# Kernel optimization log

Measured on AMD Instinct MI355X. Metric: run time of the kernel, lower is better.

The kernel has to match this reference:

```python
import jax, jax.numpy as jnp
import numpy as np

N_NODES = 50000
N_EDGES = 800000
N_GRAPHS = 128
F_IN = 128
HID = 64
EDGE_DIM = 16
H1, H2 = 4, 2
NEG_SLOPE = 0.2


def _glorot(key, shape, fan_in):
    return jax.random.normal(key, shape, dtype=jnp.float32) / np.sqrt(fan_in)


def setup_inputs() -> dict:
    key = jax.random.key(0)
    ks = jax.random.split(key, 20)
    x = jax.random.normal(ks[0], (N_NODES, F_IN), dtype=jnp.float32)
    edge_attr = jax.random.normal(ks[1], (N_EDGES, EDGE_DIM), dtype=jnp.float32)
    edge_index = jax.random.randint(ks[2], (2, N_EDGES), 0, N_NODES, dtype=jnp.int32)
    # evenly spread graph ids so every graph is non-empty (sorted)
    batch = (jnp.arange(N_NODES, dtype=jnp.int32) * N_GRAPHS) // N_NODES
    p = {
        'W1': _glorot(ks[3], (F_IN, H1 * HID), F_IN),
        'a_src1': _glorot(ks[4], (H1, HID), HID),
        'a_dst1': _glorot(ks[5], (H1, HID), HID),
        'We1': _glorot(ks[6], (EDGE_DIM, H1 * HID), EDGE_DIM),
        'a_e1': _glorot(ks[7], (H1, HID), HID),
        'b1': jnp.zeros((H1 * HID,), jnp.float32),
        'W2': _glorot(ks[8], (H1 * HID, H2 * HID), H1 * HID),
        'a_src2': _glorot(ks[9], (H2, HID), HID),
        'a_dst2': _glorot(ks[10], (H2, HID), HID),
        'We2': _glorot(ks[11], (EDGE_DIM, H2 * HID), EDGE_DIM),
        'a_e2': _glorot(ks[12], (H2, HID), HID),
        'b2': jnp.zeros((HID,), jnp.float32),
        'Wr': _glorot(ks[13], (HID, 1), HID),
        'br': jnp.zeros((1,), jnp.float32),
    }
    return dict(x=x, edge_attr=edge_attr, edge_index=edge_index, batch=batch, **p)


def _segment_softmax(scores, seg, num_segments):
    # scores: [E, H], softmax grouped by seg (destination node)
    m = jax.ops.segment_max(scores, seg, num_segments)
    m = jnp.where(jnp.isfinite(m), m, 0.0)
    ex = jnp.exp(scores - m[seg])
    s = jax.ops.segment_sum(ex, seg, num_segments)
    return ex / (s[seg] + 1e-16)


def _add_self_loops(edge_index, edge_attr, n):
    # PyG add_self_loops with fill_value='mean': per-dst mean of edge_attr
    src, dst = edge_index[0], edge_index[1]
    cnt = jax.ops.segment_sum(jnp.ones((src.shape[0],), jnp.float32), dst, n)
    loop_attr = jax.ops.segment_sum(edge_attr, dst, n) / jnp.maximum(cnt, 1.0)[:, None]
    loop = jnp.arange(n, dtype=src.dtype)
    return (jnp.concatenate([src, loop]), jnp.concatenate([dst, loop]),
            jnp.concatenate([edge_attr, loop_attr], axis=0))


def _gat_layer(x, e_attr, src, dst, W, a_src, a_dst, We, a_e, b, heads, outc, concat):
    n = x.shape[0]
    xs = (x @ W).reshape(n, heads, outc)                 # [N,H,C]
    s_src = jnp.einsum('nhc,hc->nh', xs, a_src)
    s_dst = jnp.einsum('nhc,hc->nh', xs, a_dst)
    ee = (e_attr @ We).reshape(-1, heads, outc)          # [E,H,C]
    s_e = jnp.einsum('ehc,hc->eh', ee, a_e)
    score = jax.nn.leaky_relu(s_src[src] + s_dst[dst] + s_e, NEG_SLOPE)  # [E,H]
    alpha = _segment_softmax(score, dst, n)
    out = jax.ops.segment_sum(xs[src] * alpha[..., None], dst, n)        # [N,H,C]
    out = out.reshape(n, heads * outc) if concat else out.mean(axis=1)
    return out + b


def reference(x, edge_attr, edge_index, batch,
              W1, a_src1, a_dst1, We1, a_e1, b1,
              W2, a_src2, a_dst2, We2, a_e2, b2, Wr, br):
    n = x.shape[0]
    src, dst, ea = _add_self_loops(edge_index, edge_attr, n)
    h = _gat_layer(x, ea, src, dst, W1, a_src1, a_dst1, We1, a_e1, b1, H1, HID, True)
    h = jax.nn.relu(h)
    h = _gat_layer(h, ea, src, dst, W2, a_src2, a_dst2, We2, a_e2, b2, H2, HID, False)
    g = jax.ops.segment_max(h, batch, N_GRAPHS)          # global max pool [G, HID]
    return g @ Wr + br
```

## Files before the change

kernel.cpp:

```cpp
#include <hip/hip_runtime.h>
#include <hip/hip_bf16.h>
#include <hip/hip_fp16.h>

#define DEVINL __device__ __forceinline__
typedef __hip_bfloat16 bf16;

typedef __attribute__((ext_vector_type(8))) __bf16 bf16x8;
typedef __attribute__((ext_vector_type(4))) float f32x4;

static constexpr int N_NODES  = 50000;
static constexpr int N_EDGES  = 800000;
static constexpr int N_GRAPHS = 128;
static constexpr float NEG_SLOPE = 0.2f;

DEVINL float ldIn(const void* __restrict__ p, size_t i, int isbf) {
    if (isbf) return __bfloat162float(((const bf16*)p)[i]);
    return ((const float*)p)[i];
}

DEVINL unsigned short f2bf(float f) {
    bf16 b = __float2bfloat16(f);
    return *reinterpret_cast<unsigned short*>(&b);
}

DEVINL unsigned f2hbits(float f) {
    __half h = __float2half(f);
    return (unsigned)*reinterpret_cast<unsigned short*>(&h);
}

DEVINL float hbits2f(unsigned bits) {
    unsigned short us = (unsigned short)bits;
    __half h = *reinterpret_cast<__half*>(&us);
    return __half2float(h);
}

DEVINL float lrelu_exp(float sc) {
    sc = sc > 0.f ? sc : NEG_SLOPE * sc;
    return __expf(sc);
}

DEVINL void accw(float w, unsigned wv, float& a0, float& a1) {
    a0 = fmaf(w, __uint_as_float(wv << 16), a0);
    a1 = fmaf(w, __uint_as_float(wv & 0xffff0000u), a1);
}

template<int H>
DEVINL float getse(const uint4& rv, int h) {
    unsigned bits;
    if (H == 4) {
        unsigned w16 = (h & 2) ? rv.z : rv.y;
        bits = (h & 1) ? (w16 >> 16) : (w16 & 0xffffu);
    } else {
        bits = h ? (rv.w >> 16) : (rv.w & 0xffffu);
    }
    return hbits2f(bits);
}

template<int K, int M>
DEVINL void wfrag_build(const void* __restrict__ W, int isbf,
                        bf16* __restrict__ Wfrag, int idx)
{
    constexpr int KS = K / 32;
    constexpr int total = (M / 16) * KS * 64 * 8;
    if (idx >= total) return;
    int j    = idx & 7;
    int lane = (idx >> 3) & 63;
    int rem  = idx >> 9;
    int ks   = rem % KS;
    int ct   = rem / KS;
    int k = ks * 32 + (lane >> 4) * 8 + j;
    int n = ct * 16 + (lane & 15);
    Wfrag[idx] = __float2bfloat16(ldIn(W, (size_t)k * M + n, isbf));
}

__global__ __launch_bounds__(256)
void prep_kernel(const unsigned short* __restrict__ xu,
                 const void* __restrict__ We1, const void* __restrict__ ae1,
                 const void* __restrict__ We2, const void* __restrict__ ae2,
                 const void* __restrict__ W1,  const void* __restrict__ W2,
                 int* __restrict__ flagp,
                 float* __restrict__ M1, float* __restrict__ M2,
                 bf16* __restrict__ wf1, bf16* __restrict__ wf2)
{
    __shared__ int sflag;
    const int bx = blockIdx.x;
    const int t  = threadIdx.x;
    if (t < 64) {
        int bad = 0;
        for (int i = t; i < 1024; i += 64) {
            unsigned u = xu[2 * i];
            float v = __uint_as_float(u << 16);
            if (!(fabsf(v) <= 1e4f)) bad = 1;
        }
        unsigned long long m = __ballot(bad);
        if (t == 0) sflag = m ? 0 : 1;
    }
    __syncthreads();
    const int isbf = sflag;
    if (bx == 0 && t == 0) *flagp = isbf;

    if (bx == 0) {
        if (t < 64) {
            int d = t >> 2, h = t & 3;
            float s = 0.f;
            for (int c = 0; c < 64; ++c)
                s += ldIn(We1, d * 256 + h * 64 + c, isbf) * ldIn(ae1, h * 64 + c, isbf);
            M1[d * 4 + h] = s;
        }
        if (t < 32) {
            int d = t >> 1, h = t & 1;
            float s = 0.f;
            for (int c = 0; c < 64; ++c)
                s += ldIn(We2, d * 128 + h * 64 + c, isbf) * ldIn(ae2, h * 64 + c, isbf);
            M2[d * 2 + h] = s;
        }
    } else if (bx <= 128) {
        wfrag_build<128, 256>(W1, isbf, wf1, (bx - 1) * 256 + t);
    } else {
        wfrag_build<256, 128>(W2, isbf, wf2, (bx - 129) * 256 + t);
    }
}

template<int K, int M, int AMODE, int H>
__global__ __launch_bounds__(256)
void gemm_mfma_kernel(const void* __restrict__ A, const bf16* __restrict__ Wfrag,
                      bf16* __restrict__ C, const int* __restrict__ flagp, int N,
                      const void* __restrict__ a_src, const void* __restrict__ a_dst,
                      float* __restrict__ sA, float* __restrict__ sD)
{
    constexpr int KS = K / 32, CT = M / 16;
    constexpr int LDA = K + 8;
    __shared__ __align__(16) unsigned short Asm[64 * LDA];
    const int isbf = *flagp;
    const int tid  = threadIdx.x;
    const int wave = tid >> 6, lane = tid & 63;
    const int n0 = blockIdx.x * 64;

    for (int i = tid; i < 64 * (K / 8); i += 256) {
        int r  = i / (K / 8);
        int kc = (i % (K / 8)) * 8;
        int n  = n0 + r;
        unsigned short v[8] = {0, 0, 0, 0, 0, 0, 0, 0};
        if (n < N) {
            size_t base = (size_t)n * K + kc;
            if (AMODE == 1 || isbf) {
                *reinterpret_cast<uint4*>(v) =
                    *reinterpret_cast<const uint4*>((const unsigned short*)A + base);
            } else {
                const float* Af = (const float*)A + base;
                float4 f0 = *reinterpret_cast<const float4*>(Af);
                float4 f1 = *reinterpret_cast<const float4*>(Af + 4);
                v[0] = f2bf(f0.x); v[1] = f2bf(f0.y); v[2] = f2bf(f0.z); v[3] = f2bf(f0.w);
                v[4] = f2bf(f1.x); v[5] = f2bf(f1.y); v[6] = f2bf(f1.z); v[7] = f2bf(f1.w);
            }
        }
        *reinterpret_cast<uint4*>(&Asm[r * LDA + kc]) = *reinterpret_cast<uint4*>(v);
    }
    __syncthreads();

    f32x4 acc[CT];
    #pragma unroll
    for (int ct = 0; ct < CT; ++ct) acc[ct] = (f32x4){0.f, 0.f, 0.f, 0.f};

    const int arow  = wave * 16 + (lane & 15);
    const int akoff = (lane >> 4) * 8;
    #pragma unroll
    for (int ks = 0; ks < KS; ++ks) {
        bf16x8 af = *reinterpret_cast<const bf16x8*>(&Asm[arow * LDA + ks * 32 + akoff]);
        #pragma unroll
        for (int ct = 0; ct < CT; ++ct) {
            bf16x8 bfr = *reinterpret_cast<const bf16x8*>(
                &Wfrag[(((size_t)ct * KS + ks) * 64 + lane) * 8]);
            acc[ct] = __builtin_amdgcn_mfma_f32_16x16x32_bf16(af, bfr, acc[ct], 0, 0, 0);
        }
    }

    const int crow0 = n0 + wave * 16 + (lane >> 4) * 4;
    const int ccol  = lane & 15;
    #pragma unroll
    for (int ct = 0; ct < CT; ++ct) {
        #pragma unroll
        for (int r = 0; r < 4; ++r) {
            int row = crow0 + r;
            if (row < N) C[(size_t)row * M + ct * 16 + ccol] = __float2bfloat16(acc[ct][r]);
        }
    }

    float psA[4][H], psD[4][H];
    #pragma unroll
    for (int r = 0; r < 4; ++r)
        #pragma unroll
        for (int hh = 0; hh < H; ++hh) { psA[r][hh] = 0.f; psD[r][hh] = 0.f; }
    #pragma unroll
    for (int ct = 0; ct < CT; ++ct) {
        float as = ldIn(a_src, ct * 16 + ccol, isbf);
        float ad = ldIn(a_dst, ct * 16 + ccol, isbf);
        const int hh = ct >> 2;
        #pragma unroll
        for (int r = 0; r < 4; ++r) {
            psA[r][hh] += acc[ct][r] * as;
            psD[r][hh] += acc[ct][r] * ad;
        }
    }
    #pragma unroll
    for (int m = 1; m < 16; m <<= 1) {
        #pragma unroll
        for (int r = 0; r < 4; ++r)
            #pragma unroll
            for (int hh = 0; hh < H; ++hh) {
                psA[r][hh] += __shfl_xor(psA[r][hh], m);
                psD[r][hh] += __shfl_xor(psD[r][hh], m);
            }
    }
    if (ccol == 0) {
        #pragma unroll
        for (int r = 0; r < 4; ++r) {
            int row = crow0 + r;
            if (row < N) {
                #pragma unroll
                for (int hh = 0; hh < H; ++hh) {
                    sA[(size_t)row * H + hh] = psA[r][hh];
                    sD[(size_t)row * H + hh] = psD[r][hh];
                }
            }
        }
    }
}

__global__ void csr_count_kernel(const int* __restrict__ dst, int* __restrict__ cnt,
                                 int* __restrict__ rank)
{
    int e = blockIdx.x * blockDim.x + threadIdx.x;
    if (e >= N_EDGES) return;
    rank[e] = atomicAdd(&cnt[dst[e]], 1);
}

__global__ __launch_bounds__(256)
void scan_sum_kernel(const int* __restrict__ cnt, int* __restrict__ bsum)
{
    __shared__ int sm[256];
    int i = blockIdx.x * 256 + threadIdx.x;
    sm[threadIdx.x] = (i < N_NODES) ? cnt[i] : 0;
    __syncthreads();
    for (int off = 128; off; off >>= 1) {
        if (threadIdx.x < off) sm[threadIdx.x] += sm[threadIdx.x + off];
        __syncthreads();
    }
    if (threadIdx.x == 0) bsum[blockIdx.x] = sm[0];
}

__global__ __launch_bounds__(256)
void scan_off_kernel(int* __restrict__ bsum, int nb)
{
    __shared__ int sm[256];
    int tid = threadIdx.x;
    int v = (tid < nb) ? bsum[tid] : 0;
    sm[tid] = v;
    __syncthreads();
    for (int off = 1; off < 256; off <<= 1) {
        int t = (tid >= off) ? sm[tid - off] : 0;
        __syncthreads();
        sm[tid] += t;
        __syncthreads();
    }
    if (tid < nb) bsum[tid] = sm[tid] - v;
}

__global__ __launch_bounds__(256)
void scan_final_kernel(const int* __restrict__ cnt, const int* __restrict__ bsum,
                       int* __restrict__ row)
{
    __shared__ int sm[256];
    int i = blockIdx.x * 256 + threadIdx.x;
    int tid = threadIdx.x;
    int v = (i < N_NODES) ? cnt[i] : 0;
    sm[tid] = v;
    __syncthreads();
    for (int off = 1; off < 256; off <<= 1) {
        int t = (tid >= off) ? sm[tid - off] : 0;
        __syncthreads();
        sm[tid] += t;
        __syncthreads();
    }
    int excl = sm[tid] - v + bsum[blockIdx.x];
    if (i < N_NODES) row[i] = excl;
    if (i == N_NODES - 1) row[N_NODES] = excl + v;
}

__global__ void csr_scatter_kernel(const int* __restrict__ srcI, const int* __restrict__ dstI,
                                   const void* __restrict__ eattr, const int* __restrict__ flagp,
                                   const float* __restrict__ M1, const float* __restrict__ M2,
                                   const int* __restrict__ row, const int* __restrict__ rank,
                                   uint4* __restrict__ erec)
{
    const int isbf = *flagp;
    int e = blockIdx.x * blockDim.x + threadIdx.x;
    if (e >= N_EDGES) return;
    float attr[16];
    #pragma unroll
    for (int k = 0; k < 16; ++k) attr[k] = ldIn(eattr, (size_t)e * 16 + k, isbf);
    float4 o1 = {0.f, 0.f, 0.f, 0.f};
    float2 o2 = {0.f, 0.f};
    #pragma unroll
    for (int k = 0; k < 16; ++k) {
        o1.x += attr[k] * M1[k * 4 + 0];
        o1.y += attr[k] * M1[k * 4 + 1];
        o1.z += attr[k] * M1[k * 4 + 2];
        o1.w += attr[k] * M1[k * 4 + 3];
        o2.x += attr[k] * M2[k * 2 + 0];
        o2.y += attr[k] * M2[k * 2 + 1];
    }
    int pos = row[dstI[e]] + rank[e];
    uint4 rec;
    rec.x = (unsigned)srcI[e];
    rec.y = f2hbits(o1.x) | (f2hbits(o1.y) << 16);
    rec.z = f2hbits(o1.z) | (f2hbits(o1.w) << 16);
    rec.w = f2hbits(o2.x) | (f2hbits(o2.y) << 16);
    erec[pos] = rec;
}

template<int H, int LAYER>
__global__ __launch_bounds__(256)
void agg_fused_kernel(const int* __restrict__ row, const uint4* __restrict__ erec,
                      const bf16* __restrict__ xs,
                      const float* __restrict__ sA, const float* __restrict__ sD,
                      const void* __restrict__ bias,
                      const int* __restrict__ flagp, void* __restrict__ out)
{
    constexpr int C   = H * 64;
    constexpr int CPL = C / 16;
    constexpr int NQ  = CPL / 8;
    const int isbf = *flagp;
    int dv = (blockIdx.x * 256 + threadIdx.x) >> 6;
    const int d = __builtin_amdgcn_readfirstlane(dv);
    const int lane = threadIdx.x & 63;
    if (d >= N_NODES) return;
    const int q  = lane >> 4;
    const int sl = lane & 15;
    const int h  = (sl * CPL) >> 6;
    const char* xsb = (const char*)xs;
    const unsigned lb = (unsigned)(sl * (CPL * 2));
    const float sDv = sD[(size_t)d * H + h];
    const float sAd = sA[(size_t)d * H + h];

    float acc[CPL];
    #pragma unroll
    for (int i = 0; i < CPL; ++i) acc[i] = 0.f;
    float den = 0.f, seSum = 0.f;

    const int b = row[d], eend = row[d + 1];
    const int cnt = eend - b;
    const int nb8 = cnt & ~7;

    if (nb8 > 0) {
        const int mlast = b + nb8 - 1;
        uint4 rv0 = erec[b + q];
        uint4 rv1 = erec[b + 4 + q];
        for (int j0 = b; j0 < b + nb8; j0 += 8) {
            const int s0 = (int)rv0.x, s1 = (int)rv1.x;
            const float se0 = getse<H>(rv0, h);
            const float se1 = getse<H>(rv1, h);
            const int jn = j0 + 8;
            rv0 = erec[min(jn + q, mlast)];
            rv1 = erec[min(jn + 4 + q, mlast)];
            const float sa0 = sA[(size_t)s0 * H + h];
            const float sa1 = sA[(size_t)s1 * H + h];
            const uint4* p0 = (const uint4*)(xsb + (size_t)((unsigned)s0 * (C * 2) + lb));
            const uint4* p1 = (const uint4*)(xsb + (size_t)((unsigned)s1 * (C * 2) + lb));
            uint4 xv0[NQ], xv1[NQ];
            #pragma unroll
            for (int t = 0; t < NQ; ++t) { xv0[t] = p0[t]; xv1[t] = p1[t]; }
            const float w0 = lrelu_exp(sa0 + sDv + se0);
            const float w1 = lrelu_exp(sa1 + sDv + se1);
            seSum += se0 + se1;
            den += w0 + w1;
            const unsigned* wv0 = reinterpret_cast<const unsigned*>(xv0);
            const unsigned* wv1 = reinterpret_cast<const unsigned*>(xv1);
            #pragma unroll
            for (int p = 0; p < CPL / 2; ++p) {
                accw(w0, wv0[p], acc[2 * p], acc[2 * p + 1]);
                accw(w1, wv1[p], acc[2 * p], acc[2 * p + 1]);
            }
        }
    }
    for (int j0 = b + nb8; j0 < eend; j0 += 4) {
        int jj = j0 + q;
        bool valid = jj < eend;
        int jc = valid ? jj : (eend - 1);
        uint4 rv = erec[jc];
        int s = (int)rv.x;
        float se = getse<H>(rv, h);
        float sa = sA[(size_t)s * H + h];
        const uint4* p0 = (const uint4*)(xsb + (size_t)((unsigned)s * (C * 2) + lb));
        uint4 xv[NQ];
        #pragma unroll
        for (int t = 0; t < NQ; ++t) xv[t] = p0[t];
        float w = valid ? lrelu_exp(sa + sDv + se) : 0.f;
        seSum += valid ? se : 0.f;
        den += w;
        const unsigned* wv = reinterpret_cast<const unsigned*>(xv);
        #pragma unroll
        for (int p = 0; p < CPL / 2; ++p) accw(w, wv[p], acc[2 * p], acc[2 * p + 1]);
    }

    uint4 xvS[NQ];
    {
        const uint4* pS = (const uint4*)(xsb + (size_t)((unsigned)d * (C * 2) + lb));
        #pragma unroll
        for (int t = 0; t < NQ; ++t) xvS[t] = pS[t];
    }

    #pragma unroll
    for (int i = 0; i < CPL; ++i) {
        acc[i] += __shfl_xor(acc[i], 16);
        acc[i] += __shfl_xor(acc[i], 32);
    }
    den   += __shfl_xor(den, 16);   den   += __shfl_xor(den, 32);
    seSum += __shfl_xor(seSum, 16); seSum += __shfl_xor(seSum, 32);

    {
        const float seM = seSum / fmaxf((float)cnt, 1.f);
        const float wS  = lrelu_exp(sAd + sDv + seM);
        den += wS;
        const unsigned* wv = reinterpret_cast<const unsigned*>(xvS);
        #pragma unroll
        for (int p = 0; p < CPL / 2; ++p) accw(wS, wv[p], acc[2 * p], acc[2 * p + 1]);
    }

    const float rden = 1.f / (den + 1e-16f);
    if (LAYER == 1) {
        if (q == 0) {
            unsigned o[CPL / 2];
            #pragma unroll
            for (int p = 0; p < CPL / 2; ++p) {
                float v0 = acc[2 * p] * rden + ldIn(bias, sl * CPL + 2 * p, isbf);
                float v1 = acc[2 * p + 1] * rden + ldIn(bias, sl * CPL + 2 * p + 1, isbf);
                v0 = v0 > 0.f ? v0 : 0.f;
                v1 = v1 > 0.f ? v1 : 0.f;
                o[p] = (unsigned)f2bf(v0) | ((unsigned)f2bf(v1) << 16);
            }
            uint4* op = reinterpret_cast<uint4*>(
                &((unsigned short*)out)[(size_t)d * C + sl * CPL]);
            op[0] = reinterpret_cast<uint4*>(o)[0];
            if (NQ == 2) op[1] = reinterpret_cast<uint4*>(o)[1];
        }
    } else {
        float v[CPL], pp[CPL];
        #pragma unroll
        for (int i = 0; i < CPL; ++i) {
            v[i] = acc[i] * rden;
            pp[i] = __shfl_xor(v[i], 8);
        }
        if (q == 0 && sl < 8) {
            float o[CPL];
            #pragma unroll
            for (int i = 0; i < CPL; ++i)
                o[i] = 0.5f * (v[i] + pp[i]) + ldIn(bias, sl * CPL + i, isbf);
            float4* op = reinterpret_cast<float4*>(&((float*)out)[(size_t)d * 64 + sl * CPL]);
            op[0] = reinterpret_cast<float4*>(o)[0];
            op[1] = reinterpret_cast<float4*>(o)[1];
        }
    }
}

__global__ __launch_bounds__(256)
void pool_readout_kernel(const float* __restrict__ h2, const int* __restrict__ batch,
                         const void* __restrict__ Wr, const void* __restrict__ br,
                         const int* __restrict__ flagp, void* __restrict__ out)
{
    const int isbf = *flagp;
    int gi = blockIdx.x;
    int lo = 0, hi = N_NODES;
    while (lo < hi) { int mid = (lo + hi) >> 1; if (batch[mid] < gi) lo = mid + 1; else hi = mid; }
    int start = lo;
    lo = start; hi = N_NODES;
    while (lo < hi) { int mid = (lo + hi) >> 1; if (batch[mid] < gi + 1) lo = mid + 1; else hi = mid; }
    int end = lo;
    int c = threadIdx.x & 63, chunk = threadIdx.x >> 6;
    float m = -INFINITY;
    for (int n = start + chunk; n < end; n += 4) m = fmaxf(m, h2[(size_t)n * 64 + c]);
    __shared__ float sm[256];
    sm[threadIdx.x] = m;
    __syncthreads();
    if (threadIdx.x < 64) {
        m = fmaxf(fmaxf(sm[threadIdx.x], sm[threadIdx.x + 64]),
                  fmaxf(sm[threadIdx.x + 128], sm[threadIdx.x + 192]));
        float p = m * ldIn(Wr, threadIdx.x, isbf);
        for (int off = 32; off; off >>= 1) p += __shfl_down(p, off);
        if (threadIdx.x == 0) {
            float r = p + ldIn(br, 0, isbf);
            if (isbf) ((bf16*)out)[gi] = __float2bfloat16(r);
            else      ((float*)out)[gi] = r;
        }
    }
}

extern "C" void kernel_launch(void* const* d_in, const int* in_sizes, int n_in,
                              void* d_out, int out_size, void* d_ws, size_t ws_size,
                              hipStream_t stream)
{
    const void* x     = d_in[0];
    const void* ea    = d_in[1];
    const int*  eidx  = (const int*)d_in[2];
    const int*  batch = (const int*)d_in[3];
    const void* W1  = d_in[4];
    const void* as1 = d_in[5];
    const void* ad1 = d_in[6];
    const void* We1 = d_in[7];
    const void* ae1 = d_in[8];
    const void* b1  = d_in[9];
    const void* W2  = d_in[10];
    const void* as2 = d_in[11];
    const void* ad2 = d_in[12];
    const void* We2 = d_in[13];
    const void* ae2 = d_in[14];
    const void* b2  = d_in[15];
    const void* Wr  = d_in[16];
    const void* br  = d_in[17];

    const int* srcI = eidx;
    const int* dstI = eidx + N_EDGES;

    float* ws    = (float*)d_ws;
    bf16*  xs    = (bf16*)ws;
    bf16*  h1    = (bf16*)(ws + 6400000);
    float* h2    = ws + 6400000;
    uint4* erec  = (uint4*)(ws + 12800000);
    float* sA1   = ws + 16000000;
    float* sD1   = ws + 16200000;
    float* sA2   = ws + 16400000;
    float* sD2   = ws + 16500000;
    int*   ib    = (int*)(ws + 16600000);
    int*   row    = ib;
    int*   cnt    = ib + 50016;
    int*   bsum   = ib + 100032;
    int*   rank   = ib + 100384;
    float* misc  = ws + 16600000 + 900384;
    int*   flag  = (int*)misc;
    float* M1    = misc + 16;
    float* M2    = misc + 80;
    bf16*  wf1   = (bf16*)(misc + 8320);
    bf16*  wf2   = (bf16*)(misc + 8320 + 16384);

    hipMemsetAsync(cnt, 0, N_NODES * sizeof(int), stream);

    prep_kernel<<<257, 256, 0, stream>>>((const unsigned short*)x,
                                         We1, ae1, We2, ae2, W1, W2, flag,
                                         M1, M2, wf1, wf2);

    const int NB = (N_NODES + 255) / 256;
    csr_count_kernel<<<(N_EDGES + 255) / 256, 256, 0, stream>>>(dstI, cnt, rank);
    scan_sum_kernel<<<NB, 256, 0, stream>>>(cnt, bsum);
    scan_off_kernel<<<1, 256, 0, stream>>>(bsum, NB);
    scan_final_kernel<<<NB, 256, 0, stream>>>(cnt, bsum, row);
    csr_scatter_kernel<<<(N_EDGES + 255) / 256, 256, 0, stream>>>(
        srcI, dstI, ea, flag, M1, M2, row, rank, erec);

    const int GB = (N_NODES + 63) / 64;

    gemm_mfma_kernel<128, 256, 0, 4><<<GB, 256, 0, stream>>>(
        x, wf1, xs, flag, N_NODES, as1, ad1, sA1, sD1);
    agg_fused_kernel<4, 1><<<(N_NODES + 3) / 4, 256, 0, stream>>>(
        row, erec, xs, sA1, sD1, b1, flag, h1);

    gemm_mfma_kernel<256, 128, 1, 2><<<GB, 256, 0, stream>>>(
        h1, wf2, xs, flag, N_NODES, as2, ad2, sA2, sD2);
    agg_fused_kernel<2, 2><<<(N_NODES + 3) / 4, 256, 0, stream>>>(
        row, erec, xs, sA2, sD2, b2, flag, h2);

    pool_readout_kernel<<<N_GRAPHS, 256, 0, stream>>>(h2, batch, Wr, br, flag, d_out);
}
```

Baseline: 422.5 us.

## Slice layer-1 features by column and precompute edge attention weights with atomics

After: 783.9 us. +85.5%, slower.

```diff
diff --git a/kernel.cpp b/kernel.cpp
--- a/kernel.cpp
+++ b/kernel.cpp
@@ -12,6 +12,7 @@
 static constexpr int N_EDGES  = 800000;
 static constexpr int N_GRAPHS = 128;
 static constexpr float NEG_SLOPE = 0.2f;
+static constexpr int SLICE_G = 4096;
 
 DEVINL float ldIn(const void* __restrict__ p, size_t i, int isbf) {
     if (isbf) return __bfloat162float(((const bf16*)p)[i]);
@@ -42,18 +43,6 @@
 DEVINL void accw(float w, unsigned wv, float& a0, float& a1) {
     a0 = fmaf(w, __uint_as_float(wv << 16), a0);
     a1 = fmaf(w, __uint_as_float(wv & 0xffff0000u), a1);
-}
-
-template<int H>
-DEVINL float getse(const uint4& rv, int h) {
-    unsigned bits;
-    if (H == 4) {
-        unsigned w16 = (h & 2) ? rv.z : rv.y;
-        bits = (h & 1) ? (w16 >> 16) : (w16 & 0xffffu);
-    } else {
-        bits = h ? (rv.w >> 16) : (rv.w & 0xffffu);
-    }
-    return hbits2f(bits);
 }
 
 template<int K, int M>
@@ -121,7 +110,7 @@
     }
 }
 
-template<int K, int M, int AMODE, int H>
+template<int K, int M, int AMODE, int H, int SLICED>
 __global__ __launch_bounds__(256)
 void gemm_mfma_kernel(const void* __restrict__ A, const bf16* __restrict__ Wfrag,
                       bf16* __restrict__ C, const int* __restrict__ flagp, int N,
@@ -182,7 +171,15 @@
         #pragma unroll
         for (int r = 0; r < 4; ++r) {
             int row = crow0 + r;
-            if (row < N) C[(size_t)row * M + ct * 16 + ccol] = __float2bfloat16(acc[ct][r]);
+            if (row < N) {
+                bf16 val = __float2bfloat16(acc[ct][r]);
+                if (SLICED) {
+                    int col = ct * 16 + ccol;
+                    C[(size_t)(col >> 5) * ((size_t)N * 32) + (size_t)row * 32 + (col & 31)] = val;
+                } else {
+                    C[(size_t)row * M + ct * 16 + ccol] = val;
+                }
+            }
         }
     }
 
@@ -287,11 +284,14 @@
     if (i == N_NODES - 1) row[N_NODES] = excl + v;
 }
 
-__global__ void csr_scatter_kernel(const int* __restrict__ srcI, const int* __restrict__ dstI,
-                                   const void* __restrict__ eattr, const int* __restrict__ flagp,
-                                   const float* __restrict__ M1, const float* __restrict__ M2,
-                                   const int* __restrict__ row, const int* __restrict__ rank,
-                                   uint4* __restrict__ erec)
+__global__ __launch_bounds__(256)
+void scatter_score_kernel(const int* __restrict__ srcI, const int* __restrict__ dstI,
+                          const void* __restrict__ eattr, const int* __restrict__ flagp,
+                          const float* __restrict__ M1, const float* __restrict__ M2,
+                          const int* __restrict__ row, const int* __restrict__ rank,
+                          const float* __restrict__ sA1, const float* __restrict__ sD1,
+                          unsigned* __restrict__ wrec, uint2* __restrict__ rec2,
+                          float* __restrict__ denf, float* __restrict__ seSum)
 {
     const int isbf = *flagp;
     int e = blockIdx.x * blockDim.x + threadIdx.x;
@@ -299,37 +299,132 @@
     float attr[16];
     #pragma unroll
     for (int k = 0; k < 16; ++k) attr[k] = ldIn(eattr, (size_t)e * 16 + k, isbf);
-    float4 o1 = {0.f, 0.f, 0.f, 0.f};
-    float2 o2 = {0.f, 0.f};
+    float o1a[4] = {0.f, 0.f, 0.f, 0.f};
+    float o2a[2] = {0.f, 0.f};
     #pragma unroll
     for (int k = 0; k < 16; ++k) {
-        o1.x += attr[k] * M1[k * 4 + 0];
-        o1.y += attr[k] * M1[k * 4 + 1];
-        o1.z += attr[k] * M1[k * 4 + 2];
-        o1.w += attr[k] * M1[k * 4 + 3];
-        o2.x += attr[k] * M2[k * 2 + 0];
-        o2.y += attr[k] * M2[k * 2 + 1];
-    }
-    int pos = row[dstI[e]] + rank[e];
-    uint4 rec;
-    rec.x = (unsigned)srcI[e];
-    rec.y = f2hbits(o1.x) | (f2hbits(o1.y) << 16);
-    rec.z = f2hbits(o1.z) | (f2hbits(o1.w) << 16);
-    rec.w = f2hbits(o2.x) | (f2hbits(o2.y) << 16);
-    erec[pos] = rec;
-}
-
-template<int H, int LAYER>
-__global__ __launch_bounds__(256)
-void agg_fused_kernel(const int* __restrict__ row, const uint4* __restrict__ erec,
-                      const bf16* __restrict__ xs,
-                      const float* __restrict__ sA, const float* __restrict__ sD,
-                      const void* __restrict__ bias,
-                      const int* __restrict__ flagp, void* __restrict__ out)
-{
-    constexpr int C   = H * 64;
-    constexpr int CPL = C / 16;
-    constexpr int NQ  = CPL / 8;
+        #pragma unroll
+        for (int h = 0; h < 4; ++h) o1a[h] += attr[k] * M1[k * 4 + h];
+        #pragma unroll
+        for (int h = 0; h < 2; ++h) o2a[h] += attr[k] * M2[k * 2 + h];
+    }
+    const int sidx = srcI[e];
+    const int d    = dstI[e];
+    const int pos  = row[d] + rank[e];
+    float4 sav = *reinterpret_cast<const float4*>(&sA1[(size_t)sidx * 4]);
+    float4 sdv = *reinterpret_cast<const float4*>(&sD1[(size_t)d * 4]);
+    float sa[4] = {sav.x, sav.y, sav.z, sav.w};
+    float sd[4] = {sdv.x, sdv.y, sdv.z, sdv.w};
+    #pragma unroll
+    for (int h = 0; h < 4; ++h) {
+        unsigned whb = f2hbits(lrelu_exp(sa[h] + sd[h] + o1a[h]));
+        float wr = hbits2f(whb);
+        atomicAdd(&denf[(size_t)d * 4 + h], wr);
+        atomicAdd(&seSum[(size_t)d * 4 + h], o1a[h]);
+        wrec[(size_t)h * N_EDGES + pos] = (unsigned)sidx | (whb << 16);
+    }
+    rec2[pos] = make_uint2((unsigned)sidx, f2hbits(o2a[0]) | (f2hbits(o2a[1]) << 16));
+}
+
+__global__ __launch_bounds__(256)
+void self_kernel(const int* __restrict__ cnt,
+                 const float* __restrict__ sA1, const float* __restrict__ sD1,
+                 float* __restrict__ denf, const float* __restrict__ seSum,
+                 float* __restrict__ wself)
+{
+    int i = blockIdx.x * 256 + threadIdx.x;
+    if (i >= N_NODES) return;
+    float rc = 1.f / fmaxf((float)cnt[i], 1.f);
+    float4 dv = *reinterpret_cast<const float4*>(&denf[(size_t)i * 4]);
+    float4 ss = *reinterpret_cast<const float4*>(&seSum[(size_t)i * 4]);
+    float4 sa = *reinterpret_cast<const float4*>(&sA1[(size_t)i * 4]);
+    float4 sd = *reinterpret_cast<const float4*>(&sD1[(size_t)i * 4]);
+    float w0 = lrelu_exp(sa.x + sd.x + ss.x * rc);
+    float w1 = lrelu_exp(sa.y + sd.y + ss.y * rc);
+    float w2 = lrelu_exp(sa.z + sd.z + ss.z * rc);
+    float w3 = lrelu_exp(sa.w + sd.w + ss.w * rc);
+    dv.x += w0; dv.y += w1; dv.z += w2; dv.w += w3;
+    *reinterpret_cast<float4*>(&denf[(size_t)i * 4])  = dv;
+    *reinterpret_cast<float4*>(&wself[(size_t)i * 4]) = make_float4(w0, w1, w2, w3);
+}
+
+__global__ __launch_bounds__(256)
+void slice_agg_kernel(const int* __restrict__ rowp, const unsigned* __restrict__ wrec,
+                      const bf16* __restrict__ xs, const float* __restrict__ denf,
+                      const float* __restrict__ wself, const void* __restrict__ bias,
+                      const int* __restrict__ flagp, unsigned short* __restrict__ out)
+{
+    const int isbf  = *flagp;
+    const int slice = blockIdx.x & 7;
+    const int h     = slice >> 1;
+    const int wave  = threadIdx.x >> 6;
+    const int lane  = threadIdx.x & 63;
+    const int eg    = lane >> 2;
+    const int co    = lane & 3;
+    const char* xsb = (const char*)xs + (size_t)slice * ((size_t)N_NODES * 64);
+    const unsigned* wp = wrec + (size_t)h * N_EDGES;
+
+    for (int grp = blockIdx.x >> 3; grp < (N_NODES + 3) / 4; grp += SLICE_G) {
+        const int d = __builtin_amdgcn_readfirstlane(grp * 4 + wave);
+        if (d >= N_NODES) continue;
+        const int b = rowp[d], eend = rowp[d + 1];
+
+        float acc[8];
+        #pragma unroll
+        for (int i = 0; i < 8; ++i) acc[i] = 0.f;
+
+        for (int j0 = b; j0 < eend; j0 += 16) {
+            int j = j0 + eg;
+            bool valid = j < eend;
+            int jc = valid ? j : (eend - 1);
+            unsigned wr = wp[jc];
+            int s = (int)(wr & 0xffffu);
+            float w = valid ? hbits2f(wr >> 16) : 0.f;
+            uint4 xv = *reinterpret_cast<const uint4*>(xsb + (size_t)s * 64 + co * 16);
+            const unsigned* wv = reinterpret_cast<const unsigned*>(&xv);
+            #pragma unroll
+            for (int p = 0; p < 4; ++p) accw(w, wv[p], acc[2 * p], acc[2 * p + 1]);
+        }
+
+        #pragma unroll
+        for (int i = 0; i < 8; ++i) {
+            acc[i] += __shfl_xor(acc[i], 4);
+            acc[i] += __shfl_xor(acc[i], 8);
+            acc[i] += __shfl_xor(acc[i], 16);
+            acc[i] += __shfl_xor(acc[i], 32);
+        }
+
+        const float wS   = wself[(size_t)d * 4 + h];
+        const float rden = 1.f / (denf[(size_t)d * 4 + h] + 1e-16f);
+        uint4 xvS = *reinterpret_cast<const uint4*>(xsb + (size_t)d * 64 + co * 16);
+        const unsigned* wv = reinterpret_cast<const unsigned*>(&xvS);
+        #pragma unroll
+        for (int p = 0; p < 4; ++p) accw(wS, wv[p], acc[2 * p], acc[2 * p + 1]);
+
+        if (eg == 0) {
+            unsigned o[4];
+            #pragma unroll
+            for (int p = 0; p < 4; ++p) {
+                int ch = slice * 32 + co * 8 + 2 * p;
+                float v0 = acc[2 * p] * rden + ldIn(bias, ch, isbf);
+                float v1 = acc[2 * p + 1] * rden + ldIn(bias, ch + 1, isbf);
+                v0 = v0 > 0.f ? v0 : 0.f;
+                v1 = v1 > 0.f ? v1 : 0.f;
+                o[p] = (unsigned)f2bf(v0) | ((unsigned)f2bf(v1) << 16);
+            }
+            *reinterpret_cast<uint4*>(&out[(size_t)d * 256 + slice * 32 + co * 8]) =
+                *reinterpret_cast<uint4*>(o);
+        }
+    }
+}
+
+__global__ __launch_bounds__(256)
+void agg2_kernel(const int* __restrict__ row, const uint2* __restrict__ rec2,
+                 const bf16* __restrict__ xs,
+                 const float* __restrict__ sA, const float* __restrict__ sD,
+                 const void* __restrict__ bias,
+                 const int* __restrict__ flagp, float* __restrict__ out)
+{
     const int isbf = *flagp;
     int dv = (blockIdx.x * 256 + threadIdx.x) >> 6;
     const int d = __builtin_amdgcn_readfirstlane(dv);
@@ -337,81 +432,63 @@
     if (d >= N_NODES) return;
     const int q  = lane >> 4;
     const int sl = lane & 15;
-    const int h  = (sl * CPL) >> 6;
+    const int h  = sl >> 3;
     const char* xsb = (const char*)xs;
-    const unsigned lb = (unsigned)(sl * (CPL * 2));
-    const float sDv = sD[(size_t)d * H + h];
-    const float sAd = sA[(size_t)d * H + h];
-
-    float acc[CPL];
-    #pragma unroll
-    for (int i = 0; i < CPL; ++i) acc[i] = 0.f;
+    const unsigned lb = (unsigned)(sl * 16);
+    const float sDv = sD[(size_t)d * 2 + h];
+    const float sAd = sA[(size_t)d * 2 + h];
+
+    float acc[8];
+    #pragma unroll
+    for (int i = 0; i < 8; ++i) acc[i] = 0.f;
     float den = 0.f, seSum = 0.f;
 
     const int b = row[d], eend = row[d + 1];
     const int cnt = eend - b;
     const int nb8 = cnt & ~7;
 
-    if (nb8 > 0) {
-        const int mlast = b + nb8 - 1;
-        uint4 rv0 = erec[b + q];
-        uint4 rv1 = erec[b + 4 + q];
-        for (int j0 = b; j0 < b + nb8; j0 += 8) {
-            const int s0 = (int)rv0.x, s1 = (int)rv1.x;
-            const float se0 = getse<H>(rv0, h);
-            const float se1 = getse<H>(rv1, h);
-            const int jn = j0 + 8;
-            rv0 = erec[min(jn + q, mlast)];
-            rv1 = erec[min(jn + 4 + q, mlast)];
-            const float sa0 = sA[(size_t)s0 * H + h];
-            const float sa1 = sA[(size_t)s1 * H + h];
-            const uint4* p0 = (const uint4*)(xsb + (size_t)((unsigned)s0 * (C * 2) + lb));
-            const uint4* p1 = (const uint4*)(xsb + (size_t)((unsigned)s1 * (C * 2) + lb));
-            uint4 xv0[NQ], xv1[NQ];
-            #pragma unroll
-            for (int t = 0; t < NQ; ++t) { xv0[t] = p0[t]; xv1[t] = p1[t]; }
-            const float w0 = lrelu_exp(sa0 + sDv + se0);
-            const float w1 = lrelu_exp(sa1 + sDv + se1);
-            seSum += se0 + se1;
-            den += w0 + w1;
-            const unsigned* wv0 = reinterpret_cast<const unsigned*>(xv0);
-            const unsigned* wv1 = reinterpret_cast<const unsigned*>(xv1);
-            #pragma unroll
-            for (int p = 0; p < CPL / 2; ++p) {
-                accw(w0, wv0[p], acc[2 * p], acc[2 * p + 1]);
-                accw(w1, wv1[p], acc[2 * p], acc[2 * p + 1]);
-            }
+    for (int j0 = b; j0 < b + nb8; j0 += 8) {
+        uint2 rv0 = rec2[j0 + q];
+        uint2 rv1 = rec2[j0 + 4 + q];
+        int s0 = (int)rv0.x, s1 = (int)rv1.x;
+        const uint4* p0 = (const uint4*)(xsb + (size_t)((unsigned)s0 * 256 + lb));
+        const uint4* p1 = (const uint4*)(xsb + (size_t)((unsigned)s1 * 256 + lb));
+        uint4 xv0 = *p0, xv1 = *p1;
+        float sa0 = sA[(size_t)s0 * 2 + h];
+        float sa1 = sA[(size_t)s1 * 2 + h];
+        float se0 = hbits2f(h ? (rv0.y >> 16) : (rv0.y & 0xffffu));
+        float se1 = hbits2f(h ? (rv1.y >> 16) : (rv1.y & 0xffffu));
+        float w0 = lrelu_exp(sa0 + sDv + se0);
+        float w1 = lrelu_exp(sa1 + sDv + se1);
+        seSum += se0 + se1;
+        den += w0 + w1;
+        const unsigned* wv0 = reinterpret_cast<const unsigned*>(&xv0);
+        const unsigned* wv1 = reinterpret_cast<const unsigned*>(&xv1);
+        #pragma unroll
+        for (int p = 0; p < 4; ++p) {
+            accw(w0, wv0[p], acc[2 * p], acc[2 * p + 1]);
+            accw(w1, wv1[p], acc[2 * p], acc[2 * p + 1]);
         }
     }
     for (int j0 = b + nb8; j0 < eend; j0 += 4) {
         int jj = j0 + q;
         bool valid = jj < eend;
         int jc = valid ? jj : (eend - 1);
-        uint4 rv = erec[jc];
+        uint2 rv = rec2[jc];
         int s = (int)rv.x;
-        float se = getse<H>(rv, h);
-        float sa = sA[(size_t)s * H + h];
-        const uint4* p0 = (const uint4*)(xsb + (size_t)((unsigned)s * (C * 2) + lb));
-        uint4 xv[NQ];
-        #pragma unroll
-        for (int t = 0; t < NQ; ++t) xv[t] = p0[t];
+        float se = hbits2f(h ? (rv.y >> 16) : (rv.y & 0xffffu));
+        float sa = sA[(size_t)s * 2 + h];
+        uint4 xv = *(const uint4*)(xsb + (size_t)((unsigned)s * 256 + lb));
         float w = valid ? lrelu_exp(sa + sDv + se) : 0.f;
         seSum += valid ? se : 0.f;
         den += w;
-        const unsigned* wv = reinterpret_cast<const unsigned*>(xv);
-        #pragma unroll
-        for (int p = 0; p < CPL / 2; ++p) accw(w, wv[p], acc[2 * p], acc[2 * p + 1]);
-    }
-
-    uint4 xvS[NQ];
-    {
-        const uint4* pS = (const uint4*)(xsb + (size_t)((unsigned)d * (C * 2) + lb));
-        #pragma unroll
-        for (int t = 0; t < NQ; ++t) xvS[t] = pS[t];
-    }
-
-    #pragma unroll
-    for (int i = 0; i < CPL; ++i) {
+        const unsigned* wv = reinterpret_cast<const unsigned*>(&xv);
+        #pragma unroll
+        for (int p = 0; p < 4; ++p) accw(w, wv[p], acc[2 * p], acc[2 * p + 1]);
+    }
+
+    #pragma unroll
+    for (int i = 0; i < 8; ++i) {
         acc[i] += __shfl_xor(acc[i], 16);
         acc[i] += __shfl_xor(acc[i], 32);
     }
@@ -421,45 +498,28 @@
     {
         const float seM = seSum / fmaxf((float)cnt, 1.f);
         const float wS  = lrelu_exp(sAd + sDv + seM);
+        uint4 xv = *(const uint4*)(xsb + (size_t)((unsigned)d * 256 + lb));
         den += wS;
-        const unsigned* wv = reinterpret_cast<const unsigned*>(xvS);
-        #pragma unroll
-        for (int p = 0; p < CPL / 2; ++p) accw(wS, wv[p], acc[2 * p], acc[2 * p + 1]);
+        const unsigned* wv = reinterpret_cast<const unsigned*>(&xv);
+        #pragma unroll
+        for (int p = 0; p < 4; ++p) accw(wS, wv[p], acc[2 * p], acc[2 * p + 1]);
     }
 
     const float rden = 1.f / (den + 1e-16f);
-    if (LAYER == 1) {
-        if (q == 0) {
-            unsigned o[CPL / 2];
-            #pragma unroll
-            for (int p = 0; p < CPL / 2; ++p) {
-                float v0 = acc[2 * p] * rden + ldIn(bias, sl * CPL + 2 * p, isbf);
-                float v1 = acc[2 * p + 1] * rden + ldIn(bias, sl * CPL + 2 * p + 1, isbf);
-                v0 = v0 > 0.f ? v0 : 0.f;
-                v1 = v1 > 0.f ? v1 : 0.f;
-                o[p] = (unsigned)f2bf(v0) | ((unsigned)f2bf(v1) << 16);
-            }
-            uint4* op = reinterpret_cast<uint4*>(
-                &((unsigned short*)out)[(size_t)d * C + sl * CPL]);
-            op[0] = reinterpret_cast<uint4*>(o)[0];
-            if (NQ == 2) op[1] = reinterpret_cast<uint4*>(o)[1];
-        }
-    } else {
-        float v[CPL], pp[CPL];
-        #pragma unroll
-        for (int i = 0; i < CPL; ++i) {
-            v[i] = acc[i] * rden;
-            pp[i] = __shfl_xor(v[i], 8);
-        }
-        if (q == 0 && sl < 8) {
-            float o[CPL];
-            #pragma unroll
-            for (int i = 0; i < CPL; ++i)
-                o[i] = 0.5f * (v[i] + pp[i]) + ldIn(bias, sl * CPL + i, isbf);
-            float4* op = reinterpret_cast<float4*>(&((float*)out)[(size_t)d * 64 + sl * CPL]);
-            op[0] = reinterpret_cast<float4*>(o)[0];
-            op[1] = reinterpret_cast<float4*>(o)[1];
-        }
+    float v[8], pp[8];
+    #pragma unroll
+    for (int i = 0; i < 8; ++i) {
+        v[i] = acc[i] * rden;
+        pp[i] = __shfl_xor(v[i], 8);
+    }
+    if (q == 0 && sl < 8) {
+        float o[8];
+        #pragma unroll
+        for (int i = 0; i < 8; ++i)
+            o[i] = 0.5f * (v[i] + pp[i]) + ldIn(bias, sl * 8 + i, isbf);
+        float4* op = reinterpret_cast<float4*>(&out[(size_t)d * 64 + sl * 8]);
+        op[0] = reinterpret_cast<float4*>(o)[0];
+        op[1] = reinterpret_cast<float4*>(o)[1];
     }
 }
 
@@ -525,24 +585,27 @@
     bf16*  xs    = (bf16*)ws;
     bf16*  h1    = (bf16*)(ws + 6400000);
     float* h2    = ws + 6400000;
-    uint4* erec  = (uint4*)(ws + 12800000);
-    float* sA1   = ws + 16000000;
-    float* sD1   = ws + 16200000;
-    float* sA2   = ws + 16400000;
-    float* sD2   = ws + 16500000;
-    int*   ib    = (int*)(ws + 16600000);
-    int*   row    = ib;
-    int*   cnt    = ib + 50016;
-    int*   bsum   = ib + 100032;
-    int*   rank   = ib + 100384;
-    float* misc  = ws + 16600000 + 900384;
+    uint2* rec2  = (uint2*)(ws + 12800000);
+    float* sA1   = ws + 14400000;
+    float* sD1   = ws + 14600000;
+    float* sA2   = ws + 14800000;
+    float* sD2   = ws + 14900000;
+    float* wself = ws + 15000000;
+    int*   cnt   = (int*)(ws + 15200000);
+    float* denf  = ws + 15250016;
+    float* seSum = ws + 15450016;
+    int*   row   = (int*)(ws + 15650016);
+    int*   bsum  = (int*)(ws + 15700032);
+    int*   rank  = (int*)(ws + 15700384);
+    unsigned* wrec = (unsigned*)(ws + 16500384);
+    float* misc  = ws + 19700400;
     int*   flag  = (int*)misc;
     float* M1    = misc + 16;
     float* M2    = misc + 80;
-    bf16*  wf1   = (bf16*)(misc + 8320);
-    bf16*  wf2   = (bf16*)(misc + 8320 + 16384);
-
-    hipMemsetAsync(cnt, 0, N_NODES * sizeof(int), stream);
+    bf16*  wf1   = (bf16*)(misc + 128);
+    bf16*  wf2   = (bf16*)(misc + 128 + 16384);
+
+    hipMemsetAsync(cnt, 0, 450016 * sizeof(float), stream);
 
     prep_kernel<<<257, 256, 0, stream>>>((const unsigned short*)x,
                                          We1, ae1, We2, ae2, W1, W2, flag,
@@ -553,20 +616,21 @@
     scan_sum_kernel<<<NB, 256, 0, stream>>>(cnt, bsum);
     scan_off_kernel<<<1, 256, 0, stream>>>(bsum, NB);
     scan_final_kernel<<<NB, 256, 0, stream>>>(cnt, bsum, row);
-    csr_scatter_kernel<<<(N_EDGES + 255) / 256, 256, 0, stream>>>(
-        srcI, dstI, ea, flag, M1, M2, row, rank, erec);
 
     const int GB = (N_NODES + 63) / 64;
 
-    gemm_mfma_kernel<128, 256, 0, 4><<<GB, 256, 0, stream>>>(
+    gemm_mfma_kernel<128, 256, 0, 4, 1><<<GB, 256, 0, stream>>>(
         x, wf1, xs, flag, N_NODES, as1, ad1, sA1, sD1);
-    agg_fused_kernel<4, 1><<<(N_NODES + 3) / 4, 256, 0, stream>>>(
-        row, erec, xs, sA1, sD1, b1, flag, h1);
-
-    gemm_mfma_kernel<256, 128, 1, 2><<<GB, 256, 0, stream>>>(
+    scatter_score_kernel<<<(N_EDGES + 255) / 256, 256, 0, stream>>>(
+        srcI, dstI, ea, flag, M1, M2, row, rank, sA1, sD1, wrec, rec2, denf, seSum);
+    self_kernel<<<NB, 256, 0, stream>>>(cnt, sA1, sD1, denf, seSum, wself);
+    slice_agg_kernel<<<8 * SLICE_G, 256, 0, stream>>>(
+        row, wrec, xs, denf, wself, b1, flag, (unsigned short*)h1);
+
+    gemm_mfma_kernel<256, 128, 1, 2, 0><<<GB, 256, 0, stream>>>(
         h1, wf2, xs, flag, N_NODES, as2, ad2, sA2, sD2);
-    agg_fused_kernel<2, 2><<<(N_NODES + 3) / 4, 256, 0, stream>>>(
-        row, erec, xs, sA2, sD2, b2, flag, h2);
+    agg2_kernel<<<(N_NODES + 3) / 4, 256, 0, stream>>>(
+        row, rec2, xs, sA2, sD2, b2, flag, h2);
 
     pool_readout_kernel<<<N_GRAPHS, 256, 0, stream>>>(h2, batch, Wr, br, flag, d_out);
 }
```
